# Performance work log

Hardware: AMD Instinct MI355X
Metric: run time of the kernel (lower is better)

Reference implementation:

```python
import jax, jax.numpy as jnp
import numpy as np

B, S, H, I, E = 2, 2048, 1024, 4096, 8
NUM_STEPS = 2
RMS_EPS = 1e-6


def rmsnorm(x, w, eps=RMS_EPS):
    var = jnp.mean(jnp.square(x), axis=-1, keepdims=True)
    return x * jax.lax.rsqrt(var + eps) * w


def setup_inputs() -> dict:
    key = jax.random.key(0)
    ks = jax.random.split(key, 7)
    return {
        "hidden_states": jax.random.normal(ks[0], (B, S, H), dtype=jnp.float32),
        "gate_w": jax.random.normal(ks[1], (E, H), dtype=jnp.float32) * 0.02,
        "w1": jax.random.normal(ks[2], (E, H, I), dtype=jnp.float32) * 0.02,
        "b1": jnp.zeros((E, I), dtype=jnp.float32),
        "w2": jax.random.normal(ks[3], (E, I, H), dtype=jnp.float32) * 0.02,
        "b2": jnp.zeros((E, H), dtype=jnp.float32),
        "ln_w": jnp.ones((H,), dtype=jnp.float32),
    }


def reference(hidden_states, gate_w, w1, b1, w2, b2, ln_w):
    x = hidden_states  # [B,S,H]
    dtype = hidden_states.dtype
    for i in range(NUM_STEPS):
        inp = x if i == 0 else rmsnorm(x, ln_w)
        t = inp.reshape(-1, H)  # [T,H], T = B*S
        # softmax gate (computed in fp32 as in the original)
        logits = t @ gate_w.T  # [T,E]
        rw = jax.nn.softmax(logits.astype(jnp.float32), axis=-1).astype(dtype)
        # all experts on all tokens (dense MoE), batched over E
        h = jax.nn.silu(jnp.einsum('td,edi->tei', t, w1) + b1)  # [T,E,I]
        eo = jnp.einsum('tei,eih->teh', h, w2) + b2             # [T,E,H]
        comb = jnp.einsum('te,teh->th', rw, eo)                 # weighted combine
        x = x + comb.reshape(B, S, H)
    return x  # final_projection is Identity (no feature extractor)
```

## Files before the change

### kernel.cpp

```cpp
#include <hip/hip_runtime.h>
#include <hip/hip_bf16.h>

#define T_TOK 4096
#define H_DIM 1024
#define I_DIM 4096
#define E_EXP 8
#define RMS_EPS_F 1e-6f

using bf16x8 = __attribute__((ext_vector_type(8))) __bf16;
using f32x4  = __attribute__((ext_vector_type(4))) float;

__device__ inline void gload_lds16(const void* g, void* l) {
    __builtin_amdgcn_global_load_lds(
        (const __attribute__((address_space(1))) void*)g,
        (__attribute__((address_space(3))) void*)l,
        16, 0, 0);
}

__global__ __launch_bounds__(256) void k_transpose_cvt(
    const float* __restrict__ in, __hip_bfloat16* __restrict__ out, int R, int C)
{
    __shared__ float tile[32][33];
    const size_t mat = (size_t)R * C;
    in  += (size_t)blockIdx.z * mat;
    out += (size_t)blockIdx.z * mat;
    const int c0 = blockIdx.x * 32, r0 = blockIdx.y * 32;
    const int tx = threadIdx.x & 31, ty = threadIdx.x >> 5;
#pragma unroll
    for (int dy = 0; dy < 32; dy += 8)
        tile[ty + dy][tx] = in[(size_t)(r0 + ty + dy) * C + (c0 + tx)];
    __syncthreads();
#pragma unroll
    for (int dy = 0; dy < 32; dy += 8)
        out[(size_t)(c0 + ty + dy) * R + (r0 + tx)] = __float2bfloat16(tile[tx][ty + dy]);
}

__global__ __launch_bounds__(256) void k_prep(
    const float* __restrict__ x, const float* __restrict__ lnw,
    __hip_bfloat16* __restrict__ tb, int do_norm)
{
    const int t = blockIdx.x;
    const float* row = x + (size_t)t * H_DIM;
    const int base = threadIdx.x * 4;
    float4 v = *(const float4*)(row + base);
    if (do_norm) {
        float ss = v.x*v.x + v.y*v.y + v.z*v.z + v.w*v.w;
#pragma unroll
        for (int off = 32; off > 0; off >>= 1) ss += __shfl_xor(ss, off);
        __shared__ float wsum[4];
        const int w = threadIdx.x >> 6;
        if ((threadIdx.x & 63) == 0) wsum[w] = ss;
        __syncthreads();
        const float tot = wsum[0] + wsum[1] + wsum[2] + wsum[3];
        const float scale = rsqrtf(tot * (1.0f / H_DIM) + RMS_EPS_F);
        float4 g = *(const float4*)(lnw + base);
        v.x *= scale * g.x; v.y *= scale * g.y; v.z *= scale * g.z; v.w *= scale * g.w;
    }
    __hip_bfloat16* o = tb + (size_t)t * H_DIM + base;
    o[0] = __float2bfloat16(v.x); o[1] = __float2bfloat16(v.y);
    o[2] = __float2bfloat16(v.z); o[3] = __float2bfloat16(v.w);
}

__global__ __launch_bounds__(256) void k_gate(
    const __hip_bfloat16* __restrict__ tb, const float* __restrict__ gw,
    float* __restrict__ rw)
{
    const int t = blockIdx.x * 4 + (threadIdx.x >> 6);
    const int lane = threadIdx.x & 63;
    const __hip_bfloat16* row = tb + (size_t)t * H_DIM;
    float acc[E_EXP];
#pragma unroll
    for (int e = 0; e < E_EXP; ++e) acc[e] = 0.f;
    for (int h = lane; h < H_DIM; h += 64) {
        const float xv = __bfloat162float(row[h]);
#pragma unroll
        for (int e = 0; e < E_EXP; ++e) acc[e] += xv * gw[e * H_DIM + h];
    }
#pragma unroll
    for (int e = 0; e < E_EXP; ++e) {
#pragma unroll
        for (int off = 32; off > 0; off >>= 1) acc[e] += __shfl_xor(acc[e], off);
    }
    if (lane == 0) {
        float mx = acc[0];
#pragma unroll
        for (int e = 1; e < E_EXP; ++e) mx = fmaxf(mx, acc[e]);
        float ex[E_EXP], s = 0.f;
#pragma unroll
        for (int e = 0; e < E_EXP; ++e) { ex[e] = __expf(acc[e] - mx); s += ex[e]; }
        const float inv = 1.f / s;
#pragma unroll
        for (int e = 0; e < E_EXP; ++e) rw[(size_t)t * E_EXP + e] = ex[e] * inv;
    }
}


template<int MB, int NB>
__device__ __forceinline__ void mfma_quad(const bf16x8 (&a)[4][2], const bf16x8 (&b)[4][2],
                                          f32x4 (&acc)[8][4]) {
    __builtin_amdgcn_s_setprio(1);
#pragma unroll
    for (int mi = 0; mi < 4; ++mi)
#pragma unroll
        for (int nn = 0; nn < 2; ++nn)
#pragma unroll
            for (int kc = 0; kc < 2; ++kc)
                acc[MB + mi][NB + nn] = __builtin_amdgcn_mfma_f32_16x16x32_bf16(
                    a[mi][kc], b[NB + nn][kc], acc[MB + mi][NB + nn], 0, 0, 0);
    __builtin_amdgcn_s_setprio(0);
}

template<int BB, int MBASE>
__device__ __forceinline__ void load_a4(bf16x8 (&a)[4][2], const char* rdA, int kof0, int kof1) {
#pragma unroll
    for (int mi = 0; mi < 4; ++mi) {
        a[mi][0] = *(const bf16x8*)(rdA + BB * 32768 + (MBASE + mi) * 2048 + kof0);
        a[mi][1] = *(const bf16x8*)(rdA + BB * 32768 + (MBASE + mi) * 2048 + kof1);
    }
}
template<int BB, int NBASE>
__device__ __forceinline__ void load_b2(bf16x8 (&b)[4][2], const char* rdB, int kof0, int kof1) {
#pragma unroll
    for (int ni = 0; ni < 2; ++ni) {
        b[NBASE + ni][0] = *(const bf16x8*)(rdB + BB * 32768 + (NBASE + ni) * 2048 + kof0);
        b[NBASE + ni][1] = *(const bf16x8*)(rdB + BB * 32768 + (NBASE + ni) * 2048 + kof1);
    }
}

#define BAR()   __builtin_amdgcn_s_barrier()
#define LGKM0() asm volatile("s_waitcnt lgkmcnt(0)")
#define VMW(n)  asm volatile("s_waitcnt vmcnt(" #n ")" ::: "memory")
#define SCHED0() __builtin_amdgcn_sched_barrier(0)

template <int MODE>
__global__ __launch_bounds__(512, 2) void k_gemm8(
    const __hip_bfloat16* __restrict__ A, int lda, long long strideA,
    const __hip_bfloat16* __restrict__ Bt, int ldb, long long strideB,
    const float* __restrict__ bias, int strideBias,
    void* __restrict__ out, int ldo, long long strideOut, int K)
{
    __shared__ __hip_bfloat16 sA[2][2][128 * 64];
    __shared__ __hip_bfloat16 sB[2][2][128 * 64];

    const int z = blockIdx.z;
    A  += (size_t)z * (size_t)strideA;
    Bt += (size_t)z * (size_t)strideB;

    const int tid  = threadIdx.x;
    const int lane = tid & 63;
    const int wid  = tid >> 6;
    const int wr = wid >> 2, wc = wid & 3;
    const int m0 = blockIdx.y * 256, n0 = blockIdx.x * 256;

    const int sr  = tid >> 3;
    const int skb = ((((tid & 7) * 16) ^ ((sr & 7) << 4)) >> 1);
    const __hip_bfloat16* gA = A  + (size_t)(m0 + sr) * lda + skb;
    const __hip_bfloat16* gB = Bt + (size_t)(n0 + sr) * ldb + skb;
    char* const dA = (char*)&sA[0][0][0] + tid * 16;
    char* const dB = (char*)&sB[0][0][0] + tid * 16;

#define STAGE_A(bb, hh, kt) do { \
    const __hip_bfloat16* s_ = gA + (size_t)(hh) * 128 * lda + (size_t)(kt) * 64; \
    gload_lds16(s_,                     dA + (bb) * 32768 + (hh) * 16384); \
    gload_lds16(s_ + (size_t)64 * lda,  dA + (bb) * 32768 + (hh) * 16384 + 8192); \
} while (0)
#define STAGE_B(bb, hh, kt) do { \
    const __hip_bfloat16* s_ = gB + (size_t)(hh) * 128 * ldb + (size_t)(kt) * 64; \
    gload_lds16(s_,                     dB + (bb) * 32768 + (hh) * 16384); \
    gload_lds16(s_ + (size_t)64 * ldb,  dB + (bb) * 32768 + (hh) * 16384 + 8192); \
} while (0)

    const int fr = lane & 15, kg = lane >> 4;
    const int msk  = (fr & 7) << 4;
    const int kof0 = (kg * 16) ^ msk;
    const int kof1 = (64 + kg * 16) ^ msk;
    const char* rdA = (const char*)&sA[0][wr][0] + fr * 128;
    const char* rdB = (const char*)&sB[0][wc >> 1][0] + (wc & 1) * 8192 + fr * 128;

    f32x4  acc[8][4] = {};
    bf16x8 a[4][2], b[4][2];

    const int NT = K >> 6;

    STAGE_B(0, 0, 0); STAGE_B(0, 1, 0);
    STAGE_A(0, 0, 0); STAGE_A(0, 1, 0);
    STAGE_B(1, 0, 1); STAGE_B(1, 1, 1);
    VMW(4); BAR(); SCHED0();

    for (int i = 0; i < NT / 2 - 1; ++i) {
        const int t1 = 2 * i + 1;
        load_a4<0, 0>(a, rdA, kof0, kof1);
        load_b2<0, 0>(b, rdB, kof0, kof1);
        STAGE_A(1, 0, t1);
        BAR(); LGKM0();
        mfma_quad<0, 0>(a, b, acc);
        BAR();
        load_b2<0, 2>(b, rdB, kof0, kof1);
        STAGE_A(1, 1, t1);
        BAR(); LGKM0();
        mfma_quad<0, 2>(a, b, acc);
        BAR();
        load_a4<0, 4>(a, rdA, kof0, kof1);
        STAGE_B(0, 0, t1 + 1);
        BAR(); LGKM0();
        mfma_quad<4, 0>(a, b, acc);
        BAR();
        STAGE_B(0, 1, t1 + 1);
        BAR();
        mfma_quad<4, 2>(a, b, acc);
        VMW(4); BAR(); SCHED0();
        load_a4<1, 0>(a, rdA, kof0, kof1);
        load_b2<1, 0>(b, rdB, kof0, kof1);
        STAGE_A(0, 0, t1 + 1);
        BAR(); LGKM0();
        mfma_quad<0, 0>(a, b, acc);
        BAR();
        load_b2<1, 2>(b, rdB, kof0, kof1);
        STAGE_A(0, 1, t1 + 1);
        BAR(); LGKM0();
        mfma_quad<0, 2>(a, b, acc);
        BAR();
        load_a4<1, 4>(a, rdA, kof0, kof1);
        STAGE_B(1, 0, t1 + 2);
        BAR(); LGKM0();
        mfma_quad<4, 0>(a, b, acc);
        BAR();
        STAGE_B(1, 1, t1 + 2);
        BAR();
        mfma_quad<4, 2>(a, b, acc);
        VMW(4); BAR(); SCHED0();
    }
    {
        const int t1 = NT - 1;
        load_a4<0, 0>(a, rdA, kof0, kof1);
        load_b2<0, 0>(b, rdB, kof0, kof1);
        STAGE_A(1, 0, t1);
        BAR(); LGKM0();
        mfma_quad<0, 0>(a, b, acc);
        BAR();
        load_b2<0, 2>(b, rdB, kof0, kof1);
        STAGE_A(1, 1, t1);
        BAR(); LGKM0();
        mfma_quad<0, 2>(a, b, acc);
        BAR();
        load_a4<0, 4>(a, rdA, kof0, kof1);
        BAR(); LGKM0();
        mfma_quad<4, 0>(a, b, acc);
        BAR();
        mfma_quad<4, 2>(a, b, acc);
        VMW(0); BAR(); SCHED0();
        load_a4<1, 0>(a, rdA, kof0, kof1);
        load_b2<1, 0>(b, rdB, kof0, kof1);
        BAR(); LGKM0();
        mfma_quad<0, 0>(a, b, acc);
        BAR();
        load_b2<1, 2>(b, rdB, kof0, kof1);
        BAR(); LGKM0();
        mfma_quad<0, 2>(a, b, acc);
        BAR();
        load_a4<1, 4>(a, rdA, kof0, kof1);
        BAR(); LGKM0();
        mfma_quad<4, 0>(a, b, acc);
        BAR();
        mfma_quad<4, 2>(a, b, acc);
    }

    const int rB = kg * 4;
    if (MODE == 0) {
        __hip_bfloat16* O = (__hip_bfloat16*)out + (size_t)z * (size_t)strideOut;
        const float* bz = bias + (size_t)z * (size_t)strideBias;
#pragma unroll
        for (int mi = 0; mi < 8; ++mi) {
            const int gm = m0 + wr * 128 + mi * 16 + rB;
#pragma unroll
            for (int ni = 0; ni < 4; ++ni) {
                const int gn = n0 + wc * 64 + ni * 16 + fr;
                const float bv = bz[gn];
#pragma unroll
                for (int j = 0; j < 4; ++j) {
                    float v = acc[mi][ni][j] + bv;
                    v = v / (1.f + __expf(-v));
                    O[(size_t)(gm + j) * ldo + gn] = __float2bfloat16(v);
                }
            }
        }
    } else {
        float* O = (float*)out + (size_t)z * (size_t)strideOut;
#pragma unroll
        for (int mi = 0; mi < 8; ++mi) {
            const int gm = m0 + wr * 128 + mi * 16 + rB;
#pragma unroll
            for (int ni = 0; ni < 4; ++ni) {
                const int gn = n0 + wc * 64 + ni * 16 + fr;
#pragma unroll
                for (int j = 0; j < 4; ++j)
                    O[(size_t)(gm + j) * ldo + gn] = acc[mi][ni][j];
            }
        }
    }
#undef STAGE_A
#undef STAGE_B
}

__global__ __launch_bounds__(256) void k_combine(
    const float* __restrict__ eo, const float* __restrict__ rw,
    const float* __restrict__ b2, float* __restrict__ x, int e0, int g)
{
    const int t = blockIdx.x;
    const int h = threadIdx.x * 4;
    float4 acc = *(const float4*)(x + (size_t)t * H_DIM + h);
    for (int j = 0; j < g; ++j) {
        const float w = rw[(size_t)t * E_EXP + e0 + j];
        const float4 v  = *(const float4*)(eo + ((size_t)j * T_TOK + t) * H_DIM + h);
        const float4 bz = *(const float4*)(b2 + (size_t)(e0 + j) * H_DIM + h);
        acc.x += w * (v.x + bz.x);
        acc.y += w * (v.y + bz.y);
        acc.z += w * (v.z + bz.z);
        acc.w += w * (v.w + bz.w);
    }
    *(float4*)(x + (size_t)t * H_DIM + h) = acc;
}

extern "C" void kernel_launch(void* const* d_in, const int* in_sizes, int n_in,
                              void* d_out, int out_size, void* d_ws, size_t ws_size,
                              hipStream_t stream)
{
    const float* hidden = (const float*)d_in[0];
    const float* gate_w = (const float*)d_in[1];
    const float* w1     = (const float*)d_in[2];
    const float* b1     = (const float*)d_in[3];
    const float* w2     = (const float*)d_in[4];
    const float* b2     = (const float*)d_in[5];
    const float* ln_w   = (const float*)d_in[6];
    float* x = (float*)d_out;

    const size_t w1t_b = (size_t)E_EXP * I_DIM * H_DIM * 2;
    const size_t w2t_b = (size_t)E_EXP * H_DIM * I_DIM * 2;
    const size_t tb_b  = (size_t)T_TOK * H_DIM * 2;
    const size_t rw_b  = (size_t)T_TOK * E_EXP * 4;
    const size_t hb1_b = (size_t)T_TOK * I_DIM * 2;
    const size_t eo1_b = (size_t)T_TOK * H_DIM * 4;
    const size_t base_b = w1t_b + w2t_b + tb_b + rw_b;

    int g = 0;
    for (int cand = 8; cand >= 1; cand >>= 1)
        if (base_b + (size_t)cand * (hb1_b + eo1_b) <= ws_size) { g = cand; break; }

    char* ws = (char*)d_ws;
    __hip_bfloat16* w1t = (__hip_bfloat16*)ws;  ws += w1t_b;
    __hip_bfloat16* w2t = (__hip_bfloat16*)ws;  ws += w2t_b;
    __hip_bfloat16* tb  = (__hip_bfloat16*)ws;  ws += tb_b;
    float*          rw  = (float*)ws;           ws += rw_b;
    __hip_bfloat16* hb  = (__hip_bfloat16*)ws;
    float*          eo  = (float*)(ws + (size_t)(g > 0 ? g : 1) * hb1_b);

    hipMemcpyAsync(x, hidden, (size_t)T_TOK * H_DIM * 4, hipMemcpyDeviceToDevice, stream);

    if (g == 0) return;

    k_transpose_cvt<<<dim3(I_DIM / 32, H_DIM / 32, E_EXP), 256, 0, stream>>>(w1, w1t, H_DIM, I_DIM);
    k_transpose_cvt<<<dim3(H_DIM / 32, I_DIM / 32, E_EXP), 256, 0, stream>>>(w2, w2t, I_DIM, H_DIM);

    for (int step = 0; step < 2; ++step) {
        k_prep<<<T_TOK, 256, 0, stream>>>(x, ln_w, tb, step);
        k_gate<<<T_TOK / 4, 256, 0, stream>>>(tb, gate_w, rw);

        for (int e0 = 0; e0 < E_EXP; e0 += g) {
            k_gemm8<0><<<dim3(I_DIM / 256, T_TOK / 256, g), 512, 0, stream>>>(
                tb, H_DIM, 0,
                w1t + (size_t)e0 * I_DIM * H_DIM, H_DIM, (long long)I_DIM * H_DIM,
                b1 + (size_t)e0 * I_DIM, I_DIM,
                hb, I_DIM, (long long)T_TOK * I_DIM, H_DIM);
            k_gemm8<2><<<dim3(H_DIM / 256, T_TOK / 256, g), 512, 0, stream>>>(
                hb, I_DIM, (long long)T_TOK * I_DIM,
                w2t + (size_t)e0 * H_DIM * I_DIM, I_DIM, (long long)H_DIM * I_DIM,
                nullptr, 0,
                eo, H_DIM, (long long)T_TOK * H_DIM, I_DIM);
            k_combine<<<T_TOK, 256, 0, stream>>>(eo, rw, b2, x, e0, g);
        }
    }
}
```

Before: 1.424 ms.

## Prefetch LDS fragments ahead of MFMAs and remap workgroups across XCDs

Splits the A/B register fragments into low/high halves so that all LDS reads for a K-step are issued up front and overlap the MFMA quads, removing intermediate lgkm waits and barriers. Also remaps the linear workgroup id so neighbouring tiles spread across the XCDs, and swaps the grid so M tiles iterate fastest. This aims at better L2 reuse of weight tiles. The costs are more VGPRs per thread and a remap that assumes the grid size is a multiple of 8.

```diff
diff --git a/kernel.cpp b/kernel.cpp
--- a/kernel.cpp
+++ b/kernel.cpp
@@ -96,8 +96,8 @@
 
 
 template<int MB, int NB>
-__device__ __forceinline__ void mfma_quad(const bf16x8 (&a)[4][2], const bf16x8 (&b)[4][2],
-                                          f32x4 (&acc)[8][4]) {
+__device__ __forceinline__ void mfma_q(const bf16x8 (&a)[4][2], const bf16x8 (&b)[2][2],
+                                       f32x4 (&acc)[8][4]) {
     __builtin_amdgcn_s_setprio(1);
 #pragma unroll
     for (int mi = 0; mi < 4; ++mi)
@@ -106,12 +106,12 @@
 #pragma unroll
             for (int kc = 0; kc < 2; ++kc)
                 acc[MB + mi][NB + nn] = __builtin_amdgcn_mfma_f32_16x16x32_bf16(
-                    a[mi][kc], b[NB + nn][kc], acc[MB + mi][NB + nn], 0, 0, 0);
+                    a[mi][kc], b[nn][kc], acc[MB + mi][NB + nn], 0, 0, 0);
     __builtin_amdgcn_s_setprio(0);
 }
 
 template<int BB, int MBASE>
-__device__ __forceinline__ void load_a4(bf16x8 (&a)[4][2], const char* rdA, int kof0, int kof1) {
+__device__ __forceinline__ void ld_a(bf16x8 (&a)[4][2], const char* rdA, int kof0, int kof1) {
 #pragma unroll
     for (int mi = 0; mi < 4; ++mi) {
         a[mi][0] = *(const bf16x8*)(rdA + BB * 32768 + (MBASE + mi) * 2048 + kof0);
@@ -119,11 +119,11 @@
     }
 }
 template<int BB, int NBASE>
-__device__ __forceinline__ void load_b2(bf16x8 (&b)[4][2], const char* rdB, int kof0, int kof1) {
+__device__ __forceinline__ void ld_b(bf16x8 (&b)[2][2], const char* rdB, int kof0, int kof1) {
 #pragma unroll
     for (int ni = 0; ni < 2; ++ni) {
-        b[NBASE + ni][0] = *(const bf16x8*)(rdB + BB * 32768 + (NBASE + ni) * 2048 + kof0);
-        b[NBASE + ni][1] = *(const bf16x8*)(rdB + BB * 32768 + (NBASE + ni) * 2048 + kof1);
+        b[ni][0] = *(const bf16x8*)(rdB + BB * 32768 + (NBASE + ni) * 2048 + kof0);
+        b[ni][1] = *(const bf16x8*)(rdB + BB * 32768 + (NBASE + ni) * 2048 + kof1);
     }
 }
 
@@ -142,7 +142,16 @@
     __shared__ __hip_bfloat16 sA[2][2][128 * 64];
     __shared__ __hip_bfloat16 sB[2][2][128 * 64];
 
-    const int z = blockIdx.z;
+    const int gx = gridDim.x, gy = gridDim.y;
+    const int nwg = gx * gy * gridDim.z;
+    int id = blockIdx.x + gx * (blockIdx.y + gy * blockIdx.z);
+    id = (id & 7) * (nwg >> 3) + (id >> 3);
+    const int z   = id / (gx * gy);
+    const int rem = id - z * (gx * gy);
+    const int byy = rem / gx;
+    const int bxx = rem - byy * gx;
+    const int m0 = bxx * 256, n0 = byy * 256;
+
     A  += (size_t)z * (size_t)strideA;
     Bt += (size_t)z * (size_t)strideB;
 
@@ -150,7 +159,6 @@
     const int lane = tid & 63;
     const int wid  = tid >> 6;
     const int wr = wid >> 2, wc = wid & 3;
-    const int m0 = blockIdx.y * 256, n0 = blockIdx.x * 256;
 
     const int sr  = tid >> 3;
     const int skb = ((((tid & 7) * 16) ^ ((sr & 7) << 4)) >> 1);
@@ -178,7 +186,7 @@
     const char* rdB = (const char*)&sB[0][wc >> 1][0] + (wc & 1) * 8192 + fr * 128;
 
     f32x4  acc[8][4] = {};
-    bf16x8 a[4][2], b[4][2];
+    bf16x8 aL[4][2], aH[4][2], bL[2][2], bH[2][2];
 
     const int NT = K >> 6;
 
@@ -189,80 +197,79 @@
 
     for (int i = 0; i < NT / 2 - 1; ++i) {
         const int t1 = 2 * i + 1;
-        load_a4<0, 0>(a, rdA, kof0, kof1);
-        load_b2<0, 0>(b, rdB, kof0, kof1);
+        ld_a<0, 0>(aL, rdA, kof0, kof1);
+        ld_b<0, 0>(bL, rdB, kof0, kof1);
         STAGE_A(1, 0, t1);
         BAR(); LGKM0();
-        mfma_quad<0, 0>(a, b, acc);
-        BAR();
-        load_b2<0, 2>(b, rdB, kof0, kof1);
+        ld_b<0, 2>(bH, rdB, kof0, kof1);
+        ld_a<0, 4>(aH, rdA, kof0, kof1);
+        SCHED0();
+        mfma_q<0, 0>(aL, bL, acc);
+        BAR();
         STAGE_A(1, 1, t1);
-        BAR(); LGKM0();
-        mfma_quad<0, 2>(a, b, acc);
-        BAR();
-        load_a4<0, 4>(a, rdA, kof0, kof1);
+        BAR();
+        mfma_q<0, 2>(aL, bH, acc);
+        BAR();
         STAGE_B(0, 0, t1 + 1);
-        BAR(); LGKM0();
-        mfma_quad<4, 0>(a, b, acc);
+        BAR();
+        mfma_q<4, 0>(aH, bL, acc);
         BAR();
         STAGE_B(0, 1, t1 + 1);
         BAR();
-        mfma_quad<4, 2>(a, b, acc);
+        mfma_q<4, 2>(aH, bH, acc);
         VMW(4); BAR(); SCHED0();
-        load_a4<1, 0>(a, rdA, kof0, kof1);
-        load_b2<1, 0>(b, rdB, kof0, kof1);
+        ld_a<1, 0>(aL, rdA, kof0, kof1);
+        ld_b<1, 0>(bL, rdB, kof0, kof1);
         STAGE_A(0, 0, t1 + 1);
         BAR(); LGKM0();
-        mfma_quad<0, 0>(a, b, acc);
-        BAR();
-        load_b2<1, 2>(b, rdB, kof0, kof1);
+        ld_b<1, 2>(bH, rdB, kof0, kof1);
+        ld_a<1, 4>(aH, rdA, kof0, kof1);
+        SCHED0();
+        mfma_q<0, 0>(aL, bL, acc);
+        BAR();
         STAGE_A(0, 1, t1 + 1);
-        BAR(); LGKM0();
-        mfma_quad<0, 2>(a, b, acc);
-        BAR();
-        load_a4<1, 4>(a, rdA, kof0, kof1);
+        BAR();
+        mfma_q<0, 2>(aL, bH, acc);
+        BAR();
         STAGE_B(1, 0, t1 + 2);
-        BAR(); LGKM0();
-        mfma_quad<4, 0>(a, b, acc);
+        BAR();
+        mfma_q<4, 0>(aH, bL, acc);
         BAR();
         STAGE_B(1, 1, t1 + 2);
         BAR();
-        mfma_quad<4, 2>(a, b, acc);
+        mfma_q<4, 2>(aH, bH, acc);
         VMW(4); BAR(); SCHED0();
     }
     {
         const int t1 = NT - 1;
-        load_a4<0, 0>(a, rdA, kof0, kof1);
-        load_b2<0, 0>(b, rdB, kof0, kof1);
+        ld_a<0, 0>(aL, rdA, kof0, kof1);
+        ld_b<0, 0>(bL, rdB, kof0, kof1);
         STAGE_A(1, 0, t1);
         BAR(); LGKM0();
-        mfma_quad<0, 0>(a, b, acc);
-        BAR();
-        load_b2<0, 2>(b, rdB, kof0, kof1);
+        ld_b<0, 2>(bH, rdB, kof0, kof1);
+        ld_a<0, 4>(aH, rdA, kof0, kof1);
+        SCHED0();
+        mfma_q<0, 0>(aL, bL, acc);
+        BAR();
         STAGE_A(1, 1, t1);
+        BAR();
+        mfma_q<0, 2>(aL, bH, acc);
+        BAR();
+        BAR();
+        mfma_q<4, 0>(aH, bL, acc);
+        BAR();
+        mfma_q<4, 2>(aH, bH, acc);
+        VMW(0); BAR(); SCHED0();
+        ld_a<1, 0>(aL, rdA, kof0, kof1);
+        ld_b<1, 0>(bL, rdB, kof0, kof1);
         BAR(); LGKM0();
-        mfma_quad<0, 2>(a, b, acc);
-        BAR();
-        load_a4<0, 4>(a, rdA, kof0, kof1);
-        BAR(); LGKM0();
-        mfma_quad<4, 0>(a, b, acc);
-        BAR();
-        mfma_quad<4, 2>(a, b, acc);
-        VMW(0); BAR(); SCHED0();
-        load_a4<1, 0>(a, rdA, kof0, kof1);
-        load_b2<1, 0>(b, rdB, kof0, kof1);
-        BAR(); LGKM0();
-        mfma_quad<0, 0>(a, b, acc);
-        BAR();
-        load_b2<1, 2>(b, rdB, kof0, kof1);
-        BAR(); LGKM0();
-        mfma_quad<0, 2>(a, b, acc);
-        BAR();
-        load_a4<1, 4>(a, rdA, kof0, kof1);
-        BAR(); LGKM0();
-        mfma_quad<4, 0>(a, b, acc);
-        BAR();
-        mfma_quad<4, 2>(a, b, acc);
+        ld_b<1, 2>(bH, rdB, kof0, kof1);
+        ld_a<1, 4>(aH, rdA, kof0, kof1);
+        SCHED0();
+        mfma_q<0, 0>(aL, bL, acc);
+        mfma_q<0, 2>(aL, bH, acc);
+        mfma_q<4, 0>(aH, bL, acc);
+        mfma_q<4, 2>(aH, bH, acc);
     }
 
     const int rB = kg * 4;
@@ -366,12 +373,12 @@
         k_gate<<<T_TOK / 4, 256, 0, stream>>>(tb, gate_w, rw);
 
         for (int e0 = 0; e0 < E_EXP; e0 += g) {
-            k_gemm8<0><<<dim3(I_DIM / 256, T_TOK / 256, g), 512, 0, stream>>>(
+            k_gemm8<0><<<dim3(T_TOK / 256, I_DIM / 256, g), 512, 0, stream>>>(
                 tb, H_DIM, 0,
                 w1t + (size_t)e0 * I_DIM * H_DIM, H_DIM, (long long)I_DIM * H_DIM,
                 b1 + (size_t)e0 * I_DIM, I_DIM,
                 hb, I_DIM, (long long)T_TOK * I_DIM, H_DIM);
-            k_gemm8<2><<<dim3(H_DIM / 256, T_TOK / 256, g), 512, 0, stream>>>(
+            k_gemm8<2><<<dim3(T_TOK / 256, H_DIM / 256, g), 512, 0, stream>>>(
                 hb, I_DIM, (long long)T_TOK * I_DIM,
                 w2t + (size_t)e0 * H_DIM * I_DIM, I_DIM, (long long)H_DIM * I_DIM,
                 nullptr, 0,
```

New measurement: 2.703 ms. 1.9x slower.
